# Optimization experiments

Measured on AMD Instinct MI355X. Metric: run time of the kernel, lower is better.

Reference implementation:

```python
import jax, jax.numpy as jnp
import numpy as np

EPS = 1e-6
FRAME_SEQLEN = 1560          # hardcoded in source kv-cache path
LOCAL_ATTN_SIZE = 4
MAX_ATTN = LOCAL_ATTN_SIZE * FRAME_SEQLEN  # 6240
NUM_HEADS = 12


def _ln(x, w=None, b=None):
    mu = jnp.mean(x, axis=-1, keepdims=True)
    var = jnp.mean(jnp.square(x - mu), axis=-1, keepdims=True)
    y = (x - mu) * jax.lax.rsqrt(var + EPS)
    return y * w + b if w is not None else y


def _rms(x, w):
    return x * jax.lax.rsqrt(jnp.mean(jnp.square(x), axis=-1, keepdims=True) + EPS) * w


def _rope_tables(freqs_real, freqs_imag, nf, hh, ww, start_frame, c):
    # split freqs columns into temporal / height / width parts, as in causal_rope_apply
    s0 = c - 2 * (c // 3)
    s1 = c // 3
    def build(tab):
        f0 = tab[start_frame:start_frame + nf, :s0]       # [nf, s0]
        f1 = tab[:hh, s0:s0 + s1]                          # [hh, s1]
        f2 = tab[:ww, s0 + s1:]                            # [ww, s1]
        return jnp.concatenate([
            jnp.broadcast_to(f0[:, None, None, :], (nf, hh, ww, s0)),
            jnp.broadcast_to(f1[None, :, None, :], (nf, hh, ww, s1)),
            jnp.broadcast_to(f2[None, None, :, :], (nf, hh, ww, s1)),
        ], axis=-1).reshape(nf * hh * ww, 1, c)
    return build(freqs_real), build(freqs_imag)


def _causal_rope(x, cos, sin):
    # x: [B, L, n, d] with interleaved (real, imag) pairs; cos/sin: [1, L, 1, c]
    B, L, n, d = x.shape
    c = d // 2
    xr = x.reshape(B, L, n, c, 2)
    a, b = xr[..., 0], xr[..., 1]
    out = jnp.stack([a * cos - b * sin, a * sin + b * cos], axis=-1)
    return out.reshape(B, L, n, d)


def _sdpa(q, k, v):
    scale = q.shape[-1] ** -0.5
    s = jnp.einsum('bqhd,bkhd->bhqk', q, k) * scale
    a = jax.nn.softmax(s, axis=-1)
    return jnp.einsum('bhqk,bkhd->bqhd', a, v)


def _forward(hidden_states, encoder_hidden_states, temb, freqs_real, freqs_imag,
             k_cache, v_cache, scale_shift_table,
             Wq, bq, Wk, bk, Wv, bv, Wo, bo, norm_q_w, norm_k_w,
             saln_w, saln_b,
             cWq, cbq, cWk, cbk, cWv, cbv, cWo, cbo, c_norm_q_w, c_norm_k_w,
             W1, b1, W2, b2,
             current_start, grid_h, grid_w):
    B, L, D = hidden_states.shape
    nf = temb.shape[1]
    fs = L // nf                     # == FRAME_SEQLEN
    H = NUM_HEADS
    hd = D // H
    c = hd // 2
    x = hidden_states.astype(jnp.float32)

    # AdaLN modulation per frame
    e = scale_shift_table + temb                     # [B, nf, 6, D]
    shift, scale, gate = e[:, :, 0:1], e[:, :, 1:2], e[:, :, 2:3]
    c_shift, c_scale, c_gate = e[:, :, 3:4], e[:, :, 4:5], e[:, :, 5:6]

    nh = (_ln(x).reshape(B, nf, fs, D) * (1 + scale) + shift).reshape(B, L, D)

    # self-attn projections + rms_norm_across_heads qk norm
    q = _rms(nh @ Wq.T + bq, norm_q_w).reshape(B, L, H, hd)
    k = _rms(nh @ Wk.T + bk, norm_k_w).reshape(B, L, H, hd)
    v = (nh @ Wv.T + bv).reshape(B, L, H, hd)

    # causal RoPE with temporal offset current_start // 1560
    start_frame = current_start // FRAME_SEQLEN
    cos, sin = _rope_tables(freqs_real, freqs_imag, nf, grid_h, grid_w, start_frame, c)
    cos, sin = cos[None], sin[None]                  # [1, L, 1, c]
    rq = _causal_rope(q, cos, sin)
    rk = _causal_rope(k, cos, sin)

    # kv-cache update (no-eviction branch: num_new + local_end_prev == cache size)
    kc = jax.lax.stop_gradient(k_cache).at[:, current_start:current_start + L].set(rk)
    vc = jax.lax.stop_gradient(v_cache).at[:, current_start:current_start + L].set(v)
    local_end = current_start + L
    win_lo = max(0, local_end - MAX_ATTN)
    attn = _sdpa(rq, kc[:, win_lo:local_end], vc[:, win_lo:local_end]).reshape(B, L, D)
    attn = attn @ Wo.T + bo

    # gated residual + affine LN (self_attn_residual_norm)
    x = x + (attn.reshape(B, nf, fs, D) * gate).reshape(B, L, D)
    n2 = _ln(x, saln_w, saln_b)

    # T2V cross attention
    ctx = encoder_hidden_states.astype(jnp.float32)
    Lc = ctx.shape[1]
    cq = _rms(n2 @ cWq.T + cbq, c_norm_q_w).reshape(B, L, H, hd)
    ck = _rms(ctx @ cWk.T + cbk, c_norm_k_w).reshape(B, Lc, H, hd)
    cv = (ctx @ cWv.T + cbv).reshape(B, Lc, H, hd)
    ca = _sdpa(cq, ck, cv).reshape(B, L, D) @ cWo.T + cbo

    # residual + LN with c_scale/c_shift modulation (cross_attn_residual_norm)
    x = x + ca
    n3 = (_ln(x).reshape(B, nf, fs, D) * (1 + c_scale) + c_shift).reshape(B, L, D)

    # FFN (gelu tanh) + gated residual (MulAdd)
    ff = jax.nn.gelu(n3 @ W1.T + b1, approximate=True) @ W2.T + b2
    x = x + (ff.reshape(B, nf, fs, D) * c_gate).reshape(B, L, D)
    return x


def setup_inputs() -> dict:
    key = jax.random.key(0)
    D, FF, H = 1536, 8960, NUM_HEADS
    NF, FS = 2, FRAME_SEQLEN
    L = NF * FS
    CACHE = MAX_ATTN
    CTX = 512
    hd = D // H
    c = hd // 2
    ks = iter(jax.random.split(key, 40))
    def nrm(shape, s=1.0):
        return jax.random.normal(next(ks), shape, jnp.float32) * s

    def part(dim):
        inv = 1.0 / (10000.0 ** (np.arange(0, dim, 2, dtype=np.float64) / dim))
        f = np.outer(np.arange(1024, dtype=np.float64), inv)
        return np.cos(f), np.sin(f)
    c0, s0 = part(2 * (c - 2 * (c // 3)))
    c1, s1 = part(2 * (c // 3))
    c2, s2 = part(2 * (c // 3))
    freqs_real = jnp.asarray(np.concatenate([c0, c1, c2], axis=1), jnp.float32)  # [1024, 64]
    freqs_imag = jnp.asarray(np.concatenate([s0, s1, s2], axis=1), jnp.float32)

    return dict(
        hidden_states=nrm((1, L, D)),
        encoder_hidden_states=nrm((1, CTX, D)),
        temb=nrm((1, NF, 6, D), 0.5),
        freqs_real=freqs_real, freqs_imag=freqs_imag,
        k_cache=nrm((1, CACHE, H, hd), 0.5),
        v_cache=nrm((1, CACHE, H, hd), 0.5),
        scale_shift_table=nrm((1, 6, D), D ** -0.5),
        Wq=nrm((D, D), 0.02), bq=jnp.zeros((D,), jnp.float32),
        Wk=nrm((D, D), 0.02), bk=jnp.zeros((D,), jnp.float32),
        Wv=nrm((D, D), 0.02), bv=jnp.zeros((D,), jnp.float32),
        Wo=nrm((D, D), 0.02), bo=jnp.zeros((D,), jnp.float32),
        norm_q_w=jnp.ones((D,), jnp.float32), norm_k_w=jnp.ones((D,), jnp.float32),
        saln_w=jnp.ones((D,), jnp.float32), saln_b=jnp.zeros((D,), jnp.float32),
        cWq=nrm((D, D), 0.02), cbq=jnp.zeros((D,), jnp.float32),
        cWk=nrm((D, D), 0.02), cbk=jnp.zeros((D,), jnp.float32),
        cWv=nrm((D, D), 0.02), cbv=jnp.zeros((D,), jnp.float32),
        cWo=nrm((D, D), 0.02), cbo=jnp.zeros((D,), jnp.float32),
        c_norm_q_w=jnp.ones((D,), jnp.float32), c_norm_k_w=jnp.ones((D,), jnp.float32),
        W1=nrm((FF, D), 0.02), b1=jnp.zeros((FF,), jnp.float32),
        W2=nrm((D, FF), 0.02), b2=jnp.zeros((D,), jnp.float32),
        current_start=2 * FS, grid_h=30, grid_w=52,
    )


def reference(hidden_states, encoder_hidden_states, temb, freqs_real, freqs_imag,
              k_cache, v_cache, scale_shift_table,
              Wq, bq, Wk, bk, Wv, bv, Wo, bo, norm_q_w, norm_k_w,
              saln_w, saln_b,
              cWq, cbq, cWk, cbk, cWv, cbv, cWo, cbo, c_norm_q_w, c_norm_k_w,
              W1, b1, W2, b2,
              current_start, grid_h, grid_w):
    return _forward(hidden_states, encoder_hidden_states, temb, freqs_real, freqs_imag,
                    k_cache, v_cache, scale_shift_table,
                    Wq, bq, Wk, bk, Wv, bv, Wo, bo, norm_q_w, norm_k_w,
                    saln_w, saln_b,
                    cWq, cbq, cWk, cbk, cWv, cbv, cWo, cbo, c_norm_q_w, c_norm_k_w,
                    W1, b1, W2, b2,
                    current_start, grid_h, grid_w)
```

## Files before the change

### kernel.cpp

```cpp
#include <hip/hip_runtime.h>
#include <hip/hip_bf16.h>
#include <stdint.h>

typedef uint16_t u16;
typedef uint32_t u32;
typedef float    f32x4  __attribute__((ext_vector_type(4)));
typedef __bf16   bf16x8 __attribute__((ext_vector_type(8)));
typedef u16      u16x8  __attribute__((ext_vector_type(8)));
typedef u16      u16x4  __attribute__((ext_vector_type(4)));
typedef float    f32x4v __attribute__((ext_vector_type(4)));


__device__ __forceinline__ u16 f2bf(float f) {
    u32 u = __builtin_bit_cast(u32, f);
    u32 r = u + 0x7fffu + ((u >> 16) & 1u);
    return (u16)(r >> 16);
}
__device__ __forceinline__ float bfbits2f(u32 ubits) {
    return __builtin_bit_cast(float, ubits << 16);
}
__device__ __forceinline__ u32 cvtpk(float a, float b) {
    u32 r;
    asm("v_cvt_pk_bf16_f32 %0, %1, %2" : "=v"(r) : "v"(a), "v"(b));
    return r;
}
__device__ __forceinline__ bf16x8 loadb8(const u16* p) {
    u16x8 u = *(const u16x8*)p;
    return __builtin_bit_cast(bf16x8, u);
}
__device__ __forceinline__ f32x4 mfma16(bf16x8 a, bf16x8 b, f32x4 c) {
    return __builtin_amdgcn_mfma_f32_16x16x32_bf16(a, b, c, 0, 0, 0);
}
__device__ __forceinline__ void gload16(const u16* gp, u16* lp) {
    __builtin_amdgcn_global_load_lds((const __attribute__((address_space(1))) void*)gp,
                                     (__attribute__((address_space(3))) void*)lp, 16, 0, 0);
}
__device__ __forceinline__ float blockSum(float v, volatile float* buf, int t) {
#pragma unroll
    for (int o = 1; o < 64; o <<= 1) v += __shfl_xor(v, o);
    if ((t & 63) == 0) buf[t >> 6] = v;
    __syncthreads();
    float r = buf[0] + buf[1] + buf[2] + buf[3];
    __syncthreads();
    return r;
}

struct ConvJob { const float* s; u16* d; int n4; };
struct ConvJobs { ConvJob j[12]; int cnt; };

__global__ void k_conv(ConvJobs js) {
    int tid = blockIdx.x * blockDim.x + threadIdx.x;
    int stride = gridDim.x * blockDim.x;
    for (int q = 0; q < js.cnt; q++) {
        const f32x4v* s = (const f32x4v*)js.j[q].s;
        u16x4* d = (u16x4*)js.j[q].d;
        int n4 = js.j[q].n4;
        for (int i = tid; i < n4; i += stride) {
            f32x4v v = s[i];
            u16x4 o;
            o[0] = f2bf(v[0]); o[1] = f2bf(v[1]); o[2] = f2bf(v[2]); o[3] = f2bf(v[3]);
            d[i] = o;
        }
    }
}

__global__ void k_mod(const float* __restrict__ sst, const float* __restrict__ temb, float* __restrict__ e) {
    int i = blockIdx.x * 256 + threadIdx.x;
    if (i < 18432) e[i] = sst[i % 9216] + temb[i];
}

__global__ void k_cachecvt(const float* __restrict__ kc, const float* __restrict__ vc,
                           u16* __restrict__ Ka, u16* __restrict__ Va) {
    int b = blockIdx.x;
    int hd = (b % 6) * 256 + threadIdx.x;
    int p0 = (b / 6) * 4;
    int h = hd >> 7, d = hd & 127;
    u16x4 vv;
#pragma unroll
    for (int j = 0; j < 4; j++) {
        long src = (long)(p0 + j) * 1536 + hd;
        Ka[(long)h * 798720 + (long)(p0 + j) * 128 + d] = f2bf(kc[src]);
        vv[j] = f2bf(vc[src]);
    }
    *(u16x4*)&Va[(long)h * 798720 + (long)d * 6240 + p0] = vv;
}

__global__ __launch_bounds__(256) void k_ln(const float* __restrict__ x, u16* __restrict__ out,
                                            const float* __restrict__ mulp, const float* __restrict__ addp,
                                            int perFrame, int plusOne) {
    __shared__ float buf[4];
    const int row = blockIdx.x, t = threadIdx.x;
    const float* xr = x + (long)row * 1536;
    float v[6];
    float s = 0.f;
#pragma unroll
    for (int k = 0; k < 6; k++) { v[k] = xr[t + k * 256]; s += v[k]; }
    s = blockSum(s, buf, t);
    float mu = s * (1.f / 1536.f);
    float q = 0.f;
#pragma unroll
    for (int k = 0; k < 6; k++) { float d = v[k] - mu; q += d * d; }
    q = blockSum(q, buf, t);
    float inv = rsqrtf(q * (1.f / 1536.f) + 1e-6f);
    const int fo = perFrame ? (row / 1560) * 9216 : 0;
    u16* orow = out + (long)row * 1536;
    float add1 = plusOne ? 1.f : 0.f;
#pragma unroll
    for (int k = 0; k < 6; k++) {
        int c = t + k * 256;
        float m = mulp[fo + c] + add1;
        float y = (v[k] - mu) * inv * m + addp[fo + c];
        orow[c] = f2bf(y);
    }
}

__global__ __launch_bounds__(256) void k_rmsrope(const u16* __restrict__ in, int ld, int colOff,
                                                 const float* __restrict__ bias,
                                                 const float* __restrict__ w,
                                                 u16* __restrict__ out, long headStride,
                                                 const float* __restrict__ fr, const float* __restrict__ fi,
                                                 int doRope) {
    __shared__ float buf[4];
    const int row = blockIdx.x, t = threadIdx.x;
    const u32* xr = (const u32*)(in + (long)row * ld + colOff);
    const float2* b2 = (const float2*)bias;
    float px[3], py[3];
    float ss = 0.f;
#pragma unroll
    for (int i = 0; i < 3; i++) {
        u32 u = xr[t * 3 + i];
        float2 bb = b2[t * 3 + i];
        px[i] = bfbits2f(u & 0xffffu) + bb.x;
        py[i] = bfbits2f(u >> 16) + bb.y;
        ss += px[i] * px[i] + py[i] * py[i];
    }
    ss = blockSum(ss, buf, t);
    float inv = rsqrtf(ss * (1.f / 1536.f) + 1e-6f);
    int frame = 0, gh = 0, gw = 0;
    if (doRope) { frame = row / 1560; int rem = row - frame * 1560; gh = rem / 52; gw = rem - gh * 52; }
    const float2* w2 = (const float2*)w;
#pragma unroll
    for (int i = 0; i < 3; i++) {
        int jg = t * 3 + i;
        int hh = jg >> 6, j = jg & 63;
        float2 ww = w2[jg];
        float a = px[i] * inv * ww.x, b = py[i] * inv * ww.y;
        float oa = a, ob = b;
        if (doRope) {
            int fidx = (j < 22) ? (2 + frame) : ((j < 43) ? gh : gw);
            float cs = fr[fidx * 64 + j], sn = fi[fidx * 64 + j];
            oa = a * cs - b * sn;
            ob = a * sn + b * cs;
        }
        u16* dst = out + (long)hh * headStride + (long)row * 128 + j * 2;
        dst[0] = f2bf(oa);
        dst[1] = f2bf(ob);
    }
}

__global__ void k_scatterT(const u16* __restrict__ in, int ld, int colOff,
                           const float* __restrict__ bias, u16* __restrict__ outT,
                           int kvLen, int posOff) {
    int hd = blockIdx.x * 256 + threadIdx.x;
    int r0 = blockIdx.y * 4;
    int h = hd >> 7, d = hd & 127;
    float bi = bias[hd];
    u16x4 pk;
#pragma unroll
    for (int j = 0; j < 4; j++)
        pk[j] = f2bf(bfbits2f(in[(long)(r0 + j) * ld + colOff + hd]) + bi);
    *(u16x4*)&outT[(long)h * 128 * kvLen + (long)d * kvLen + posOff + r0] = pk;
}

struct GemmP {
    const u16* A; const u16* B; void* C;
    const float* bias; const float* gate; const float* resid;
    int M, N, K, ldA, ldB, ldC, kChunk;
};

template <int EPI>
__global__ __launch_bounds__(256) void k_gemm(GemmP g) {
    __shared__ alignas(16) u16 As[128 * 32];
    __shared__ alignas(16) u16 Bs[128 * 32];
    const int t = threadIdx.x;
    const int w = t >> 6, l = t & 63, lr = l & 15, lg = l >> 4;
    const int wm = w >> 1, wn = w & 1;
    const long m0 = (long)blockIdx.y * 128, n0 = (long)blockIdx.x * 128;
    f32x4 acc[4][4];
#pragma unroll
    for (int a = 0; a < 4; a++)
#pragma unroll
        for (int b = 0; b < 4; b++) acc[a][b] = f32x4{0.f, 0.f, 0.f, 0.f};

    const int rowU = t >> 2, c8 = t & 3;
    long arow[2], brow[2];
#pragma unroll
    for (int i = 0; i < 2; i++) {
        long r = m0 + rowU + i * 64;
        if (r > (long)g.M - 1) r = g.M - 1;
        arow[i] = r;
        brow[i] = n0 + rowU + i * 64;
    }

    const int kBeg = blockIdx.z * g.kChunk;
    const int kEnd = min(g.K, kBeg + g.kChunk);
    for (int k0 = kBeg; k0 < kEnd; k0 += 32) {
        __syncthreads();
#pragma unroll
        for (int i = 0; i < 2; i++) {
            gload16(g.A + arow[i] * (long)g.ldA + k0 + c8 * 8, &As[(i * 256 + w * 64) * 8]);
            gload16(g.B + brow[i] * (long)g.ldB + k0 + c8 * 8, &Bs[(i * 256 + w * 64) * 8]);
        }
        __syncthreads();
        bf16x8 am[4], bn[4];
#pragma unroll
        for (int mi = 0; mi < 4; mi++) am[mi] = loadb8(&As[(wm * 64 + mi * 16 + lr) * 32 + lg * 8]);
#pragma unroll
        for (int ni = 0; ni < 4; ni++) bn[ni] = loadb8(&Bs[(wn * 64 + ni * 16 + lr) * 32 + lg * 8]);
#pragma unroll
        for (int mi = 0; mi < 4; mi++)
#pragma unroll
            for (int ni = 0; ni < 4; ni++)
                acc[mi][ni] = mfma16(am[mi], bn[ni], acc[mi][ni]);
    }

#pragma unroll
    for (int mi = 0; mi < 4; mi++) {
#pragma unroll
        for (int ni = 0; ni < 4; ni++) {
            long col = n0 + wn * 64 + ni * 16 + lr;
            float bi = g.bias ? g.bias[col] : 0.f;
#pragma unroll
            for (int r = 0; r < 4; r++) {
                long row = m0 + wm * 64 + mi * 16 + lg * 4 + r;
                if (row >= g.M) continue;
                float v = acc[mi][ni][r] + bi;
                if constexpr (EPI == 0) {
                    ((float*)g.C)[row * g.ldC + col] = v;
                } else if constexpr (EPI == 1) {
                    ((u16*)g.C)[row * g.ldC + col] = f2bf(v);
                } else if constexpr (EPI == 2) {
                    float x3 = v * v * v;
                    float gl = 0.5f * v * (1.f + tanhf(0.79788456080286536f * (v + 0.044715f * x3)));
                    ((u16*)g.C)[row * g.ldC + col] = f2bf(gl);
                } else if constexpr (EPI == 3) {
                    float gt = g.gate ? g.gate[(row / 1560) * 9216 + col] : 1.f;
                    ((float*)g.C)[row * g.ldC + col] = g.resid[row * g.ldC + col] + v * gt;
                } else {
                    ((float*)g.C)[(long)blockIdx.z * ((long)g.M * g.ldC) + row * g.ldC + col] = v;
                }
            }
        }
    }
}

__global__ void k_gcomb(const float* __restrict__ P, int S, long MN4,
                        const float* __restrict__ bias, const float* __restrict__ gate,
                        const float* __restrict__ resid, float* __restrict__ out) {
    long i = (long)blockIdx.x * 256 + threadIdx.x;
    if (i >= MN4) return;
    f32x4v a = ((const f32x4v*)P)[i];
#pragma unroll 3
    for (int s = 1; s < S; s++) {
        f32x4v b = ((const f32x4v*)P)[(long)s * MN4 + i];
        a[0] += b[0]; a[1] += b[1]; a[2] += b[2]; a[3] += b[3];
    }
    long e0 = i * 4;
    int col = (int)(e0 % 1536);
    int fo = (int)((e0 / 1536) / 1560) * 9216;
    f32x4v r = ((const f32x4v*)resid)[i];
#pragma unroll
    for (int j = 0; j < 4; j++)
        r[j] += (a[j] + bias[col + j]) * gate[fo + col + j];
    ((f32x4v*)out)[i] = r;
}

__global__ __launch_bounds__(256) void k_flash(const u16* __restrict__ Qb, const u16* __restrict__ Kb,
                                               const u16* __restrict__ Vtg,
                                               u16* __restrict__ Opart, float2* __restrict__ ms,
                                               int kvLen, int qlen, int splitIters, int totIters) {
    __shared__ alignas(16) u16 Kt[32 * 136];
    __shared__ alignas(16) u16 Vt[128 * 40];
    __shared__ alignas(16) u16 Pt[4][32 * 40];
    const int t = threadIdx.x;
    const int w = t >> 6, l = t & 63, lr = l & 15, lg = l >> 4;
    const int head = blockIdx.y, z = blockIdx.z;
    const long q0 = (long)blockIdx.x * 128;
    const u16* Qh = Qb + (long)head * qlen * 128;
    const u16* Kh = Kb + (long)head * kvLen * 128;
    const u16* Vh = Vtg + (long)head * kvLen * 128;
    constexpr float SCL2 = 0.08838834764831845f * 1.44269504088896f;

    bf16x8 aq[2][4];
#pragma unroll
    for (int wq = 0; wq < 2; wq++)
#pragma unroll
        for (int c = 0; c < 4; c++) {
            long row = q0 + w * 32 + wq * 16 + lr;
            if (row > (long)qlen - 1) row = qlen - 1;
            aq[wq][c] = loadb8(Qh + row * 128 + c * 32 + lg * 8);
        }

    f32x4 o[2][8];
    float mrow[2] = {-1e30f, -1e30f}, srow[2] = {0.f, 0.f};
#pragma unroll
    for (int wq = 0; wq < 2; wq++)
#pragma unroll
        for (int db = 0; db < 8; db++) o[wq][db] = f32x4{0.f, 0.f, 0.f, 0.f};

    const int kr = t >> 4, c16 = (t & 15) * 8;
    const int vr = t >> 1, vh = (t & 1) * 16;

    const int it0 = z * splitIters;
    const int itN = min(totIters, it0 + splitIters);
    for (int kt = it0; kt < itN; kt++) {
        const long k0 = (long)kt * 32;
        __syncthreads();
        {
            u16x8 a0 = *(const u16x8*)(Kh + (k0 + kr) * 128 + c16);
            u16x8 a1 = *(const u16x8*)(Kh + (k0 + kr + 16) * 128 + c16);
            *(u16x8*)&Kt[kr * 136 + c16] = a0;
            *(u16x8*)&Kt[(kr + 16) * 136 + c16] = a1;
            u16x8 b0 = *(const u16x8*)(Vh + (long)vr * kvLen + k0 + vh);
            u16x8 b1 = *(const u16x8*)(Vh + (long)vr * kvLen + k0 + vh + 8);
            *(u16x8*)&Vt[vr * 40 + vh] = b0;
            *(u16x8*)&Vt[vr * 40 + vh + 8] = b1;
        }
        __syncthreads();

        f32x4 s[2][2];
#pragma unroll
        for (int kh = 0; kh < 2; kh++) {
            bf16x8 kf[4];
#pragma unroll
            for (int cb = 0; cb < 4; cb++)
                kf[cb] = loadb8(&Kt[(kh * 16 + lr) * 136 + cb * 32 + lg * 8]);
#pragma unroll
            for (int wq = 0; wq < 2; wq++) {
                f32x4 acc = f32x4{0.f, 0.f, 0.f, 0.f};
#pragma unroll
                for (int cb = 0; cb < 4; cb++) acc = mfma16(kf[cb], aq[wq][cb], acc);
                s[wq][kh] = acc;
            }
        }

#pragma unroll
        for (int wq = 0; wq < 2; wq++) {
            float pm = fmaxf(fmaxf(fmaxf(s[wq][0][0], s[wq][0][1]), fmaxf(s[wq][0][2], s[wq][0][3])),
                             fmaxf(fmaxf(s[wq][1][0], s[wq][1][1]), fmaxf(s[wq][1][2], s[wq][1][3])));
            pm = fmaxf(pm, __shfl_xor(pm, 16));
            pm = fmaxf(pm, __shfl_xor(pm, 32));
            float pm2 = pm * SCL2;
            if (__any(pm2 > mrow[wq] + 8.f)) {
                float nm = fmaxf(mrow[wq], pm2);
                float fsc = exp2f(mrow[wq] - nm);
                mrow[wq] = nm;
                srow[wq] *= fsc;
#pragma unroll
                for (int db = 0; db < 8; db++) {
                    f32x4 t4 = o[wq][db];
                    t4[0] *= fsc; t4[1] *= fsc; t4[2] *= fsc; t4[3] *= fsc;
                    o[wq][db] = t4;
                }
            }
            float p[8];
#pragma unroll
            for (int kh = 0; kh < 2; kh++)
#pragma unroll
                for (int r = 0; r < 4; r++)
                    p[kh * 4 + r] = exp2f(fmaf(s[wq][kh][r], SCL2, -mrow[wq]));
            float ts = ((p[0] + p[1]) + (p[2] + p[3])) + ((p[4] + p[5]) + (p[6] + p[7]));
            ts += __shfl_xor(ts, 16);
            ts += __shfl_xor(ts, 32);
            srow[wq] += ts;
            u32 w0 = cvtpk(p[0], p[1]), w1 = cvtpk(p[2], p[3]);
            u32 w2 = cvtpk(p[4], p[5]), w3 = cvtpk(p[6], p[7]);
            u16* pp = &Pt[w][(wq * 16 + lr) * 40 + lg * 4];
            *(u32*)pp = w0;
            *(u32*)(pp + 2) = w1;
            *(u32*)(pp + 16) = w2;
            *(u32*)(pp + 18) = w3;
        }

        bf16x8 pb0 = loadb8(&Pt[w][lr * 40 + lg * 8]);
        bf16x8 pb1 = loadb8(&Pt[w][(16 + lr) * 40 + lg * 8]);
#pragma unroll
        for (int db = 0; db < 8; db++) {
            bf16x8 vf = loadb8(&Vt[(db * 16 + lr) * 40 + lg * 8]);
            o[0][db] = mfma16(vf, pb0, o[0][db]);
            o[1][db] = mfma16(vf, pb1, o[1][db]);
        }
    }

    const long part = ((long)z * 12 + head) * qlen;
#pragma unroll
    for (int wq = 0; wq < 2; wq++) {
        long row = q0 + w * 32 + wq * 16 + lr;
        if (row < qlen) {
            if (lg == 0) {
                float2 v; v.x = mrow[wq]; v.y = srow[wq];
                ms[part + row] = v;
            }
#pragma unroll
            for (int db = 0; db < 8; db++) {
                u16x4 pk;
#pragma unroll
                for (int r = 0; r < 4; r++) pk[r] = f2bf(o[wq][db][r]);
                *(u16x4*)&Opart[(part + row) * 128 + db * 16 + lg * 4] = pk;
            }
        }
    }
}

__global__ __launch_bounds__(256) void k_combine(const u16* __restrict__ Opart, const float2* __restrict__ ms,
                                                 u16* __restrict__ Ob, int qlen, int S) {
    int idx = blockIdx.x * 4 + (threadIdx.x >> 6);
    int l = threadIdx.x & 63;
    int h = idx / qlen, q = idx - h * qlen;
    float2 mm[6];
    float M = -1e30f;
    for (int s = 0; s < S; s++) {
        mm[s] = ms[((long)s * 12 + h) * qlen + q];
        M = fmaxf(M, mm[s].x);
    }
    float den = 0.f, a0 = 0.f, a1 = 0.f;
    for (int s = 0; s < S; s++) {
        float wgt = exp2f(mm[s].x - M);
        den += wgt * mm[s].y;
        u32 two = *(const u32*)&Opart[(((long)s * 12 + h) * qlen + q) * 128 + l * 2];
        a0 += wgt * bfbits2f(two & 0xffffu);
        a1 += wgt * bfbits2f(two >> 16);
    }
    float inv = 1.f / den;
    u32 o = ((u32)f2bf(a1 * inv) << 16) | (u32)f2bf(a0 * inv);
    *(u32*)&Ob[(long)q * 1536 + h * 128 + l * 2] = o;
}

extern "C" void kernel_launch(void* const* d_in, const int* in_sizes, int n_in,
                              void* d_out, int out_size, void* d_ws, size_t ws_size,
                              hipStream_t stream) {
    const float* hs    = (const float*)d_in[0];
    const float* ctx   = (const float*)d_in[1];
    const float* temb  = (const float*)d_in[2];
    const float* fr    = (const float*)d_in[3];
    const float* fi    = (const float*)d_in[4];
    const float* kcache= (const float*)d_in[5];
    const float* vcache= (const float*)d_in[6];
    const float* sst   = (const float*)d_in[7];
    const float* Wq = (const float*)d_in[8],  *bq = (const float*)d_in[9];
    const float* Wk = (const float*)d_in[10], *bk = (const float*)d_in[11];
    const float* Wv = (const float*)d_in[12], *bv = (const float*)d_in[13];
    const float* Wo = (const float*)d_in[14], *bo = (const float*)d_in[15];
    const float* nqw = (const float*)d_in[16], *nkw = (const float*)d_in[17];
    const float* salnw = (const float*)d_in[18], *salnb = (const float*)d_in[19];
    const float* cWq = (const float*)d_in[20], *cbq = (const float*)d_in[21];
    const float* cWk = (const float*)d_in[22], *cbk = (const float*)d_in[23];
    const float* cWv = (const float*)d_in[24], *cbv = (const float*)d_in[25];
    const float* cWo = (const float*)d_in[26], *cbo = (const float*)d_in[27];
    const float* cnqw = (const float*)d_in[28], *cnkw = (const float*)d_in[29];
    const float* W1 = (const float*)d_in[30], *b1 = (const float*)d_in[31];
    const float* W2 = (const float*)d_in[32], *b2 = (const float*)d_in[33];
    float* out = (float*)d_out;

    char* base = (char*)d_ws;
    size_t off = 0;
    auto alloc = [&](size_t bytes) -> char* {
        char* p = base + off;
        off = (off + bytes + 255) & ~(size_t)255;
        return p;
    };
    float* e   = (float*)alloc(18432 * 4);
    u16* nbuf  = (u16*)alloc((size_t)3120 * 1536 * 2);
    u16* lin   = (u16*)alloc((size_t)3120 * 4608 * 2);
    u16* Qb    = (u16*)alloc((size_t)12 * 3120 * 128 * 2);
    u16* Ka    = (u16*)alloc((size_t)12 * 6240 * 128 * 2);
    u16* Va    = (u16*)alloc((size_t)12 * 6240 * 128 * 2);
    u16* attnb = (u16*)alloc((size_t)3120 * 1536 * 2);
    float* X1  = (float*)alloc((size_t)3120 * 1536 * 4);
    u16* CKb   = (u16*)alloc((size_t)12 * 512 * 128 * 2);
    u16* CVt   = (u16*)alloc((size_t)12 * 512 * 128 * 2);
    u16* H1    = (u16*)alloc((size_t)3120 * 8960 * 2);
    u16* wqkv_b= (u16*)alloc((size_t)4608 * 1536 * 2);
    u16* wo_b  = (u16*)alloc((size_t)1536 * 1536 * 2);
    u16* cwq_b = (u16*)alloc((size_t)1536 * 1536 * 2);
    u16* cwkv_b= (u16*)alloc((size_t)3072 * 1536 * 2);
    u16* cwo_b = (u16*)alloc((size_t)1536 * 1536 * 2);
    u16* w1_b  = (u16*)alloc((size_t)8960 * 1536 * 2);
    u16* w2_b  = (u16*)alloc((size_t)8960 * 1536 * 2);
    u16* ctxb  = (u16*)alloc((size_t)512 * 1536 * 2);

    u16* Opart = H1;
    float2* msb = (float2*)lin;
    float* pbuf = (float*)lin;

    ConvJobs cj{};
    auto setj = [&](int i, const float* s, u16* d, int n) { cj.j[i].s = s; cj.j[i].d = d; cj.j[i].n4 = n / 4; };
    setj(0, Wq, wqkv_b, 1536 * 1536);
    setj(1, Wk, wqkv_b + (size_t)1536 * 1536, 1536 * 1536);
    setj(2, Wv, wqkv_b + (size_t)2 * 1536 * 1536, 1536 * 1536);
    setj(3, Wo, wo_b, 1536 * 1536);
    setj(4, cWq, cwq_b, 1536 * 1536);
    setj(5, cWk, cwkv_b, 1536 * 1536);
    setj(6, cWv, cwkv_b + (size_t)1536 * 1536, 1536 * 1536);
    setj(7, cWo, cwo_b, 1536 * 1536);
    setj(8, W1, w1_b, 8960 * 1536);
    setj(9, W2, w2_b, 8960 * 1536);
    setj(10, ctx, ctxb, 512 * 1536);
    cj.cnt = 11;
    k_conv<<<2048, 256, 0, stream>>>(cj);

    k_mod<<<72, 256, 0, stream>>>(sst, temb, e);
    k_cachecvt<<<4680, 256, 0, stream>>>(kcache, vcache, Ka, Va);

    k_ln<<<3120, 256, 0, stream>>>(hs, nbuf, e + 1536, e + 0, 1, 1);

    GemmP gqkv{nbuf, wqkv_b, lin, nullptr, nullptr, nullptr, 3120, 4608, 1536, 1536, 1536, 4608, 1536};
    k_gemm<1><<<dim3(36, 25), 256, 0, stream>>>(gqkv);
    k_rmsrope<<<3120, 256, 0, stream>>>(lin, 4608, 0, bq, nqw, Qb, (long)3120 * 128, fr, fi, 1);
    k_rmsrope<<<3120, 256, 0, stream>>>(lin, 4608, 1536, bk, nkw, Ka + (size_t)3120 * 128, (long)6240 * 128, fr, fi, 1);
    k_scatterT<<<dim3(6, 780), 256, 0, stream>>>(lin, 4608, 3072, bv, Va, 6240, 3120);

    k_flash<<<dim3(25, 12, 5), 256, 0, stream>>>(Qb, Ka, Va, Opart, msb, 6240, 3120, 39, 195);
    k_combine<<<9360, 256, 0, stream>>>(Opart, msb, attnb, 3120, 5);

    GemmP gwo{attnb, wo_b, X1, bo, e + 2 * 1536, hs, 3120, 1536, 1536, 1536, 1536, 1536, 1536};
    k_gemm<3><<<dim3(12, 25), 256, 0, stream>>>(gwo);

    k_ln<<<3120, 256, 0, stream>>>(X1, nbuf, salnw, salnb, 0, 0);

    GemmP gcq{nbuf, cwq_b, lin, nullptr, nullptr, nullptr, 3120, 1536, 1536, 1536, 1536, 1536, 1536};
    k_gemm<1><<<dim3(12, 25), 256, 0, stream>>>(gcq);
    k_rmsrope<<<3120, 256, 0, stream>>>(lin, 1536, 0, cbq, cnqw, Qb, (long)3120 * 128, fr, fi, 0);

    GemmP gckv{ctxb, cwkv_b, lin, nullptr, nullptr, nullptr, 512, 3072, 1536, 1536, 1536, 3072, 1536};
    k_gemm<1><<<dim3(24, 4), 256, 0, stream>>>(gckv);
    k_rmsrope<<<512, 256, 0, stream>>>(lin, 3072, 0, cbk, cnkw, CKb, (long)512 * 128, fr, fi, 0);
    k_scatterT<<<dim3(6, 128), 256, 0, stream>>>(lin, 3072, 1536, cbv, CVt, 512, 0);

    k_flash<<<dim3(25, 12, 4), 256, 0, stream>>>(Qb, CKb, CVt, Opart, msb, 512, 3120, 4, 16);
    k_combine<<<9360, 256, 0, stream>>>(Opart, msb, attnb, 3120, 4);

    GemmP gcwo{attnb, cwo_b, X1, cbo, nullptr, X1, 3120, 1536, 1536, 1536, 1536, 1536, 1536};
    k_gemm<3><<<dim3(12, 25), 256, 0, stream>>>(gcwo);

    k_ln<<<3120, 256, 0, stream>>>(X1, nbuf, e + 4 * 1536, e + 3 * 1536, 1, 1);

    GemmP g1{nbuf, w1_b, H1, b1, nullptr, nullptr, 3120, 8960, 1536, 1536, 1536, 8960, 1536};
    k_gemm<2><<<dim3(70, 25), 256, 0, stream>>>(g1);

    GemmP g2{H1, w2_b, pbuf, nullptr, nullptr, nullptr, 3120, 1536, 8960, 8960, 8960, 1536, 2240};
    k_gemm<5><<<dim3(12, 25, 4), 256, 0, stream>>>(g2);
    k_gcomb<<<4680, 256, 0, stream>>>(pbuf, 4, 1198080, b2, e + 5 * 1536, X1, out);
}
```

Before: 1.170 ms.

## Pipeline flash attention with 64-wide KV tiles, smaller GEMM tiles, split-K cross KV

The flash kernel now processes 64-key tiles. It prefetches the next K/V tile into registers while computing the current one, and raises MFMA priority with s_setprio. The KV cache is padded to a stride of 6272, and the tail is zeroed and masked so that 6240 keys split evenly into 64-wide tiles. The GEMM becomes templated on BM so the 1536-wide output projections use 64-row tiles for more blocks. The small cross-attention KV GEMM switches to split-K with a new reduction kernel. Together these aim to hide global-load latency in attention and to improve occupancy on under-filled GEMMs, at the cost of extra launches, more register pressure and padding memory.

```diff
diff --git a/kernel.cpp b/kernel.cpp
--- a/kernel.cpp
+++ b/kernel.cpp
@@ -10,6 +10,8 @@
 typedef u16      u16x4  __attribute__((ext_vector_type(4)));
 typedef float    f32x4v __attribute__((ext_vector_type(4)));
 
+#define KSTR 6272
+#define KHS  802816
 
 __device__ __forceinline__ u16 f2bf(float f) {
     u32 u = __builtin_bit_cast(u32, f);
@@ -79,10 +81,17 @@
 #pragma unroll
     for (int j = 0; j < 4; j++) {
         long src = (long)(p0 + j) * 1536 + hd;
-        Ka[(long)h * 798720 + (long)(p0 + j) * 128 + d] = f2bf(kc[src]);
+        Ka[(long)h * KHS + (long)(p0 + j) * 128 + d] = f2bf(kc[src]);
         vv[j] = f2bf(vc[src]);
     }
-    *(u16x4*)&Va[(long)h * 798720 + (long)d * 6240 + p0] = vv;
+    *(u16x4*)&Va[(long)h * KHS + (long)d * KSTR + p0] = vv;
+}
+
+__global__ void k_zpad(u16* __restrict__ Ka, u16* __restrict__ Va) {
+    int i = blockIdx.x * 256 + threadIdx.x;
+    int h = i >> 12, rem = i & 4095, row = rem >> 7, d = rem & 127;
+    Ka[(long)h * KHS + (long)(6240 + row) * 128 + d] = 0;
+    Va[(long)h * KHS + (long)d * KSTR + 6240 + row] = 0;
 }
 
 __global__ __launch_bounds__(256) void k_ln(const float* __restrict__ x, u16* __restrict__ out,
@@ -160,7 +169,7 @@
 
 __global__ void k_scatterT(const u16* __restrict__ in, int ld, int colOff,
                            const float* __restrict__ bias, u16* __restrict__ outT,
-                           int kvLen, int posOff) {
+                           int vstride, int posOff) {
     int hd = blockIdx.x * 256 + threadIdx.x;
     int r0 = blockIdx.y * 4;
     int h = hd >> 7, d = hd & 127;
@@ -169,7 +178,7 @@
 #pragma unroll
     for (int j = 0; j < 4; j++)
         pk[j] = f2bf(bfbits2f(in[(long)(r0 + j) * ld + colOff + hd]) + bi);
-    *(u16x4*)&outT[(long)h * 128 * kvLen + (long)d * kvLen + posOff + r0] = pk;
+    *(u16x4*)&outT[(long)h * 128 * vstride + (long)d * vstride + posOff + r0] = pk;
 }
 
 struct GemmP {
@@ -178,17 +187,19 @@
     int M, N, K, ldA, ldB, ldC, kChunk;
 };
 
-template <int EPI>
+template <int EPI, int BM>
 __global__ __launch_bounds__(256) void k_gemm(GemmP g) {
-    __shared__ alignas(16) u16 As[128 * 32];
+    constexpr int WM = BM / 2;
+    constexpr int TM = BM / 32;
+    __shared__ alignas(16) u16 As[BM * 32];
     __shared__ alignas(16) u16 Bs[128 * 32];
     const int t = threadIdx.x;
     const int w = t >> 6, l = t & 63, lr = l & 15, lg = l >> 4;
     const int wm = w >> 1, wn = w & 1;
-    const long m0 = (long)blockIdx.y * 128, n0 = (long)blockIdx.x * 128;
-    f32x4 acc[4][4];
-#pragma unroll
-    for (int a = 0; a < 4; a++)
+    const long m0 = (long)blockIdx.y * BM, n0 = (long)blockIdx.x * 128;
+    f32x4 acc[TM][4];
+#pragma unroll
+    for (int a = 0; a < TM; a++)
 #pragma unroll
         for (int b = 0; b < 4; b++) acc[a][b] = f32x4{0.f, 0.f, 0.f, 0.f};
 
@@ -207,32 +218,33 @@
     for (int k0 = kBeg; k0 < kEnd; k0 += 32) {
         __syncthreads();
 #pragma unroll
-        for (int i = 0; i < 2; i++) {
+        for (int i = 0; i < BM / 64; i++)
             gload16(g.A + arow[i] * (long)g.ldA + k0 + c8 * 8, &As[(i * 256 + w * 64) * 8]);
+#pragma unroll
+        for (int i = 0; i < 2; i++)
             gload16(g.B + brow[i] * (long)g.ldB + k0 + c8 * 8, &Bs[(i * 256 + w * 64) * 8]);
-        }
         __syncthreads();
-        bf16x8 am[4], bn[4];
-#pragma unroll
-        for (int mi = 0; mi < 4; mi++) am[mi] = loadb8(&As[(wm * 64 + mi * 16 + lr) * 32 + lg * 8]);
+        bf16x8 am[TM], bn[4];
+#pragma unroll
+        for (int mi = 0; mi < TM; mi++) am[mi] = loadb8(&As[(wm * WM + mi * 16 + lr) * 32 + lg * 8]);
 #pragma unroll
         for (int ni = 0; ni < 4; ni++) bn[ni] = loadb8(&Bs[(wn * 64 + ni * 16 + lr) * 32 + lg * 8]);
 #pragma unroll
-        for (int mi = 0; mi < 4; mi++)
+        for (int mi = 0; mi < TM; mi++)
 #pragma unroll
             for (int ni = 0; ni < 4; ni++)
                 acc[mi][ni] = mfma16(am[mi], bn[ni], acc[mi][ni]);
     }
 
 #pragma unroll
-    for (int mi = 0; mi < 4; mi++) {
+    for (int mi = 0; mi < TM; mi++) {
 #pragma unroll
         for (int ni = 0; ni < 4; ni++) {
             long col = n0 + wn * 64 + ni * 16 + lr;
             float bi = g.bias ? g.bias[col] : 0.f;
 #pragma unroll
             for (int r = 0; r < 4; r++) {
-                long row = m0 + wm * 64 + mi * 16 + lg * 4 + r;
+                long row = m0 + wm * WM + mi * 16 + lg * 4 + r;
                 if (row >= g.M) continue;
                 float v = acc[mi][ni][r] + bi;
                 if constexpr (EPI == 0) {
@@ -275,20 +287,35 @@
     ((f32x4v*)out)[i] = r;
 }
 
+__global__ void k_sumbf(const float* __restrict__ P, int S, long N4, u16* __restrict__ out) {
+    long i = (long)blockIdx.x * 256 + threadIdx.x;
+    if (i >= N4) return;
+    f32x4v a = ((const f32x4v*)P)[i];
+#pragma unroll 3
+    for (int s = 1; s < S; s++) {
+        f32x4v b = ((const f32x4v*)P)[(long)s * N4 + i];
+        a[0] += b[0]; a[1] += b[1]; a[2] += b[2]; a[3] += b[3];
+    }
+    u16x4 o;
+    o[0] = f2bf(a[0]); o[1] = f2bf(a[1]); o[2] = f2bf(a[2]); o[3] = f2bf(a[3]);
+    ((u16x4*)out)[i] = o;
+}
+
 __global__ __launch_bounds__(256) void k_flash(const u16* __restrict__ Qb, const u16* __restrict__ Kb,
                                                const u16* __restrict__ Vtg,
                                                u16* __restrict__ Opart, float2* __restrict__ ms,
-                                               int kvLen, int qlen, int splitIters, int totIters) {
-    __shared__ alignas(16) u16 Kt[32 * 136];
-    __shared__ alignas(16) u16 Vt[128 * 40];
+                                               int kvStride, int kvLen, int qlen,
+                                               int splitIters, int totIters) {
+    __shared__ alignas(16) u16 Kt[64 * 136];
+    __shared__ alignas(16) u16 Vt[128 * 72];
     __shared__ alignas(16) u16 Pt[4][32 * 40];
     const int t = threadIdx.x;
     const int w = t >> 6, l = t & 63, lr = l & 15, lg = l >> 4;
     const int head = blockIdx.y, z = blockIdx.z;
     const long q0 = (long)blockIdx.x * 128;
     const u16* Qh = Qb + (long)head * qlen * 128;
-    const u16* Kh = Kb + (long)head * kvLen * 128;
-    const u16* Vh = Vtg + (long)head * kvLen * 128;
+    const u16* Kh = Kb + (long)head * (long)kvStride * 128;
+    const u16* Vh = Vtg + (long)head * (long)kvStride * 128;
     constexpr float SCL2 = 0.08838834764831845f * 1.44269504088896f;
 
     bf16x8 aq[2][4];
@@ -308,88 +335,118 @@
 #pragma unroll
         for (int db = 0; db < 8; db++) o[wq][db] = f32x4{0.f, 0.f, 0.f, 0.f};
 
-    const int kr = t >> 4, c16 = (t & 15) * 8;
-    const int vr = t >> 1, vh = (t & 1) * 16;
+    const int krow = t >> 2, kcol = (t & 3) * 32;
+    const int vrow = t >> 1, vcol = (t & 1) * 32;
+    u16x8 pkr[4], pvr[4];
 
     const int it0 = z * splitIters;
     const int itN = min(totIters, it0 + splitIters);
+
+    auto loadTile = [&](int kt) {
+        long k0 = (long)kt * 64;
+        const u16* kp = Kh + (k0 + krow) * 128 + kcol;
+#pragma unroll
+        for (int j = 0; j < 4; j++) pkr[j] = *(const u16x8*)(kp + j * 8);
+        const u16* vp = Vh + (long)vrow * kvStride + k0 + vcol;
+#pragma unroll
+        for (int j = 0; j < 4; j++) pvr[j] = *(const u16x8*)(vp + j * 8);
+    };
+    auto writeTile = [&]() {
+#pragma unroll
+        for (int j = 0; j < 4; j++) *(u16x8*)&Kt[krow * 136 + kcol + j * 8] = pkr[j];
+#pragma unroll
+        for (int j = 0; j < 4; j++) *(u16x8*)&Vt[vrow * 72 + vcol + j * 8] = pvr[j];
+    };
+
+    loadTile(it0);
+    writeTile();
+    __syncthreads();
+
     for (int kt = it0; kt < itN; kt++) {
-        const long k0 = (long)kt * 32;
-        __syncthreads();
-        {
-            u16x8 a0 = *(const u16x8*)(Kh + (k0 + kr) * 128 + c16);
-            u16x8 a1 = *(const u16x8*)(Kh + (k0 + kr + 16) * 128 + c16);
-            *(u16x8*)&Kt[kr * 136 + c16] = a0;
-            *(u16x8*)&Kt[(kr + 16) * 136 + c16] = a1;
-            u16x8 b0 = *(const u16x8*)(Vh + (long)vr * kvLen + k0 + vh);
-            u16x8 b1 = *(const u16x8*)(Vh + (long)vr * kvLen + k0 + vh + 8);
-            *(u16x8*)&Vt[vr * 40 + vh] = b0;
-            *(u16x8*)&Vt[vr * 40 + vh + 8] = b1;
+        const bool hasNext = (kt + 1 < itN);
+        if (hasNext) loadTile(kt + 1);
+        const int lim = kvLen - kt * 64;
+
+#pragma unroll
+        for (int h2 = 0; h2 < 2; h2++) {
+            f32x4 s[2][2];
+            __builtin_amdgcn_s_setprio(1);
+#pragma unroll
+            for (int kh = 0; kh < 2; kh++) {
+                bf16x8 kf[4];
+#pragma unroll
+                for (int cb = 0; cb < 4; cb++)
+                    kf[cb] = loadb8(&Kt[(h2 * 32 + kh * 16 + lr) * 136 + cb * 32 + lg * 8]);
+#pragma unroll
+                for (int wq = 0; wq < 2; wq++) {
+                    f32x4 acc = f32x4{0.f, 0.f, 0.f, 0.f};
+#pragma unroll
+                    for (int cb = 0; cb < 4; cb++) acc = mfma16(kf[cb], aq[wq][cb], acc);
+                    s[wq][kh] = acc;
+                }
+            }
+            __builtin_amdgcn_s_setprio(0);
+
+            const int sublim = lim - h2 * 32;
+#pragma unroll
+            for (int wq = 0; wq < 2; wq++) {
+                float pm = fmaxf(fmaxf(fmaxf(s[wq][0][0], s[wq][0][1]), fmaxf(s[wq][0][2], s[wq][0][3])),
+                                 fmaxf(fmaxf(s[wq][1][0], s[wq][1][1]), fmaxf(s[wq][1][2], s[wq][1][3])));
+                pm = fmaxf(pm, __shfl_xor(pm, 16));
+                pm = fmaxf(pm, __shfl_xor(pm, 32));
+                float pm2 = pm * SCL2;
+                if (__any(pm2 > mrow[wq] + 8.f)) {
+                    float nm = fmaxf(mrow[wq], pm2);
+                    float fsc = exp2f(mrow[wq] - nm);
+                    mrow[wq] = nm;
+                    srow[wq] *= fsc;
+#pragma unroll
+                    for (int db = 0; db < 8; db++) {
+                        f32x4 t4 = o[wq][db];
+                        t4[0] *= fsc; t4[1] *= fsc; t4[2] *= fsc; t4[3] *= fsc;
+                        o[wq][db] = t4;
+                    }
+                }
+                float p[8];
+#pragma unroll
+                for (int kh = 0; kh < 2; kh++)
+#pragma unroll
+                    for (int r = 0; r < 4; r++)
+                        p[kh * 4 + r] = exp2f(fmaf(s[wq][kh][r], SCL2, -mrow[wq]));
+                if (sublim < 32) {
+#pragma unroll
+                    for (int kh = 0; kh < 2; kh++)
+#pragma unroll
+                        for (int r = 0; r < 4; r++)
+                            if (kh * 16 + lg * 4 + r >= sublim) p[kh * 4 + r] = 0.f;
+                }
+                float ts = ((p[0] + p[1]) + (p[2] + p[3])) + ((p[4] + p[5]) + (p[6] + p[7]));
+                ts += __shfl_xor(ts, 16);
+                ts += __shfl_xor(ts, 32);
+                srow[wq] += ts;
+                u32 w0 = cvtpk(p[0], p[1]), w1 = cvtpk(p[2], p[3]);
+                u32 w2 = cvtpk(p[4], p[5]), w3 = cvtpk(p[6], p[7]);
+                u16* pp = &Pt[w][(wq * 16 + lr) * 40 + lg * 4];
+                *(u32*)pp = w0;
+                *(u32*)(pp + 2) = w1;
+                *(u32*)(pp + 16) = w2;
+                *(u32*)(pp + 18) = w3;
+            }
+
+            bf16x8 pb0 = loadb8(&Pt[w][lr * 40 + lg * 8]);
+            bf16x8 pb1 = loadb8(&Pt[w][(16 + lr) * 40 + lg * 8]);
+            __builtin_amdgcn_s_setprio(1);
+#pragma unroll
+            for (int db = 0; db < 8; db++) {
+                bf16x8 vf = loadb8(&Vt[(db * 16 + lr) * 72 + h2 * 32 + lg * 8]);
+                o[0][db] = mfma16(vf, pb0, o[0][db]);
+                o[1][db] = mfma16(vf, pb1, o[1][db]);
+            }
+            __builtin_amdgcn_s_setprio(0);
         }
         __syncthreads();
-
-        f32x4 s[2][2];
-#pragma unroll
-        for (int kh = 0; kh < 2; kh++) {
-            bf16x8 kf[4];
-#pragma unroll
-            for (int cb = 0; cb < 4; cb++)
-                kf[cb] = loadb8(&Kt[(kh * 16 + lr) * 136 + cb * 32 + lg * 8]);
-#pragma unroll
-            for (int wq = 0; wq < 2; wq++) {
-                f32x4 acc = f32x4{0.f, 0.f, 0.f, 0.f};
-#pragma unroll
-                for (int cb = 0; cb < 4; cb++) acc = mfma16(kf[cb], aq[wq][cb], acc);
-                s[wq][kh] = acc;
-            }
-        }
-
-#pragma unroll
-        for (int wq = 0; wq < 2; wq++) {
-            float pm = fmaxf(fmaxf(fmaxf(s[wq][0][0], s[wq][0][1]), fmaxf(s[wq][0][2], s[wq][0][3])),
-                             fmaxf(fmaxf(s[wq][1][0], s[wq][1][1]), fmaxf(s[wq][1][2], s[wq][1][3])));
-            pm = fmaxf(pm, __shfl_xor(pm, 16));
-            pm = fmaxf(pm, __shfl_xor(pm, 32));
-            float pm2 = pm * SCL2;
-            if (__any(pm2 > mrow[wq] + 8.f)) {
-                float nm = fmaxf(mrow[wq], pm2);
-                float fsc = exp2f(mrow[wq] - nm);
-                mrow[wq] = nm;
-                srow[wq] *= fsc;
-#pragma unroll
-                for (int db = 0; db < 8; db++) {
-                    f32x4 t4 = o[wq][db];
-                    t4[0] *= fsc; t4[1] *= fsc; t4[2] *= fsc; t4[3] *= fsc;
-                    o[wq][db] = t4;
-                }
-            }
-            float p[8];
-#pragma unroll
-            for (int kh = 0; kh < 2; kh++)
-#pragma unroll
-                for (int r = 0; r < 4; r++)
-                    p[kh * 4 + r] = exp2f(fmaf(s[wq][kh][r], SCL2, -mrow[wq]));
-            float ts = ((p[0] + p[1]) + (p[2] + p[3])) + ((p[4] + p[5]) + (p[6] + p[7]));
-            ts += __shfl_xor(ts, 16);
-            ts += __shfl_xor(ts, 32);
-            srow[wq] += ts;
-            u32 w0 = cvtpk(p[0], p[1]), w1 = cvtpk(p[2], p[3]);
-            u32 w2 = cvtpk(p[4], p[5]), w3 = cvtpk(p[6], p[7]);
-            u16* pp = &Pt[w][(wq * 16 + lr) * 40 + lg * 4];
-            *(u32*)pp = w0;
-            *(u32*)(pp + 2) = w1;
-            *(u32*)(pp + 16) = w2;
-            *(u32*)(pp + 18) = w3;
-        }
-
-        bf16x8 pb0 = loadb8(&Pt[w][lr * 40 + lg * 8]);
-        bf16x8 pb1 = loadb8(&Pt[w][(16 + lr) * 40 + lg * 8]);
-#pragma unroll
-        for (int db = 0; db < 8; db++) {
-            bf16x8 vf = loadb8(&Vt[(db * 16 + lr) * 40 + lg * 8]);
-            o[0][db] = mfma16(vf, pb0, o[0][db]);
-            o[1][db] = mfma16(vf, pb1, o[1][db]);
-        }
+        if (hasNext) writeTile();
+        __syncthreads();
     }
 
     const long part = ((long)z * 12 + head) * qlen;
@@ -473,8 +530,8 @@
     u16* nbuf  = (u16*)alloc((size_t)3120 * 1536 * 2);
     u16* lin   = (u16*)alloc((size_t)3120 * 4608 * 2);
     u16* Qb    = (u16*)alloc((size_t)12 * 3120 * 128 * 2);
-    u16* Ka    = (u16*)alloc((size_t)12 * 6240 * 128 * 2);
-    u16* Va    = (u16*)alloc((size_t)12 * 6240 * 128 * 2);
+    u16* Ka    = (u16*)alloc((size_t)12 * KSTR * 128 * 2);
+    u16* Va    = (u16*)alloc((size_t)12 * KSTR * 128 * 2);
     u16* attnb = (u16*)alloc((size_t)3120 * 1536 * 2);
     float* X1  = (float*)alloc((size_t)3120 * 1536 * 4);
     u16* CKb   = (u16*)alloc((size_t)12 * 512 * 128 * 2);
@@ -492,6 +549,7 @@
     u16* Opart = H1;
     float2* msb = (float2*)lin;
     float* pbuf = (float*)lin;
+    float* cpart = (float*)H1;
 
     ConvJobs cj{};
     auto setj = [&](int i, const float* s, u16* d, int n) { cj.j[i].s = s; cj.j[i].d = d; cj.j[i].n4 = n / 4; };
@@ -511,44 +569,46 @@
 
     k_mod<<<72, 256, 0, stream>>>(sst, temb, e);
     k_cachecvt<<<4680, 256, 0, stream>>>(kcache, vcache, Ka, Va);
+    k_zpad<<<192, 256, 0, stream>>>(Ka, Va);
 
     k_ln<<<3120, 256, 0, stream>>>(hs, nbuf, e + 1536, e + 0, 1, 1);
 
     GemmP gqkv{nbuf, wqkv_b, lin, nullptr, nullptr, nullptr, 3120, 4608, 1536, 1536, 1536, 4608, 1536};
-    k_gemm<1><<<dim3(36, 25), 256, 0, stream>>>(gqkv);
+    k_gemm<1, 128><<<dim3(36, 25), 256, 0, stream>>>(gqkv);
     k_rmsrope<<<3120, 256, 0, stream>>>(lin, 4608, 0, bq, nqw, Qb, (long)3120 * 128, fr, fi, 1);
-    k_rmsrope<<<3120, 256, 0, stream>>>(lin, 4608, 1536, bk, nkw, Ka + (size_t)3120 * 128, (long)6240 * 128, fr, fi, 1);
-    k_scatterT<<<dim3(6, 780), 256, 0, stream>>>(lin, 4608, 3072, bv, Va, 6240, 3120);
-
-    k_flash<<<dim3(25, 12, 5), 256, 0, stream>>>(Qb, Ka, Va, Opart, msb, 6240, 3120, 39, 195);
+    k_rmsrope<<<3120, 256, 0, stream>>>(lin, 4608, 1536, bk, nkw, Ka + (size_t)3120 * 128, (long)KHS, fr, fi, 1);
+    k_scatterT<<<dim3(6, 780), 256, 0, stream>>>(lin, 4608, 3072, bv, Va, KSTR, 3120);
+
+    k_flash<<<dim3(25, 12, 5), 256, 0, stream>>>(Qb, Ka, Va, Opart, msb, KSTR, 6240, 3120, 20, 98);
     k_combine<<<9360, 256, 0, stream>>>(Opart, msb, attnb, 3120, 5);
 
     GemmP gwo{attnb, wo_b, X1, bo, e + 2 * 1536, hs, 3120, 1536, 1536, 1536, 1536, 1536, 1536};
-    k_gemm<3><<<dim3(12, 25), 256, 0, stream>>>(gwo);
+    k_gemm<3, 64><<<dim3(12, 49), 256, 0, stream>>>(gwo);
 
     k_ln<<<3120, 256, 0, stream>>>(X1, nbuf, salnw, salnb, 0, 0);
 
     GemmP gcq{nbuf, cwq_b, lin, nullptr, nullptr, nullptr, 3120, 1536, 1536, 1536, 1536, 1536, 1536};
-    k_gemm<1><<<dim3(12, 25), 256, 0, stream>>>(gcq);
+    k_gemm<1, 64><<<dim3(12, 49), 256, 0, stream>>>(gcq);
     k_rmsrope<<<3120, 256, 0, stream>>>(lin, 1536, 0, cbq, cnqw, Qb, (long)3120 * 128, fr, fi, 0);
 
-    GemmP gckv{ctxb, cwkv_b, lin, nullptr, nullptr, nullptr, 512, 3072, 1536, 1536, 1536, 3072, 1536};
-    k_gemm<1><<<dim3(24, 4), 256, 0, stream>>>(gckv);
+    GemmP gckv{ctxb, cwkv_b, cpart, nullptr, nullptr, nullptr, 512, 3072, 1536, 1536, 1536, 3072, 384};
+    k_gemm<5, 64><<<dim3(24, 8, 4), 256, 0, stream>>>(gckv);
+    k_sumbf<<<1536, 256, 0, stream>>>(cpart, 4, 393216, lin);
     k_rmsrope<<<512, 256, 0, stream>>>(lin, 3072, 0, cbk, cnkw, CKb, (long)512 * 128, fr, fi, 0);
     k_scatterT<<<dim3(6, 128), 256, 0, stream>>>(lin, 3072, 1536, cbv, CVt, 512, 0);
 
-    k_flash<<<dim3(25, 12, 4), 256, 0, stream>>>(Qb, CKb, CVt, Opart, msb, 512, 3120, 4, 16);
+    k_flash<<<dim3(25, 12, 4), 256, 0, stream>>>(Qb, CKb, CVt, Opart, msb, 512, 512, 3120, 2, 8);
     k_combine<<<9360, 256, 0, stream>>>(Opart, msb, attnb, 3120, 4);
 
     GemmP gcwo{attnb, cwo_b, X1, cbo, nullptr, X1, 3120, 1536, 1536, 1536, 1536, 1536, 1536};
-    k_gemm<3><<<dim3(12, 25), 256, 0, stream>>>(gcwo);
+    k_gemm<3, 64><<<dim3(12, 49), 256, 0, stream>>>(gcwo);
 
     k_ln<<<3120, 256, 0, stream>>>(X1, nbuf, e + 4 * 1536, e + 3 * 1536, 1, 1);
 
     GemmP g1{nbuf, w1_b, H1, b1, nullptr, nullptr, 3120, 8960, 1536, 1536, 1536, 8960, 1536};
-    k_gemm<2><<<dim3(70, 25), 256, 0, stream>>>(g1);
+    k_gemm<2, 128><<<dim3(70, 25), 256, 0, stream>>>(g1);
 
     GemmP g2{H1, w2_b, pbuf, nullptr, nullptr, nullptr, 3120, 1536, 8960, 8960, 8960, 1536, 2240};
-    k_gemm<5><<<dim3(12, 25, 4), 256, 0, stream>>>(g2);
+    k_gemm<5, 128><<<dim3(12, 25, 4), 256, 0, stream>>>(g2);
     k_gcomb<<<4680, 256, 0, stream>>>(pbuf, 4, 1198080, b2, e + 5 * 1536, X1, out);
 }
```

Result: slower. 1.278 ms (+9.2%).
